# Kernel tuning notes

Hardware: AMD Instinct MI355X
Metric: run time of the kernel (lower is better)

## Reference

```python
import jax, jax.numpy as jnp
import numpy as np

B, N, C = 16, 1024, 768
D = 512
DEPTH = 4
K = 3
HP = WP = 32
A_EPS = 1e-4
POW_MIN = 1e-20
LN_EPS = 1e-5


def setup_inputs() -> dict:
    key = jax.random.key(0)
    ks = jax.random.split(key, 20)
    inp = {
        "tokens": jax.random.normal(ks[0], (B, N, C), dtype=jnp.float32),
        "in_proj_w": jax.random.normal(ks[1], (C, D), dtype=jnp.float32) * 0.02,
        "in_proj_b": jnp.zeros((D,), dtype=jnp.float32),
        "blk_norm_w": jnp.ones((DEPTH, D), dtype=jnp.float32),
        "blk_norm_b": jnp.zeros((DEPTH, D), dtype=jnp.float32),
        "blk_inp_w": jax.random.normal(ks[2], (DEPTH, D, 2 * D), dtype=jnp.float32) * 0.02,
        "blk_inp_b": jnp.zeros((DEPTH, 2 * D), dtype=jnp.float32),
        "blk_conv_w": jax.random.normal(ks[3], (DEPTH, K, K, 1, D), dtype=jnp.float32) * 0.1,
        "blk_conv_b": jnp.zeros((DEPTH, D), dtype=jnp.float32),
        "blk_a_logit": jax.random.normal(ks[4], (DEPTH, D), dtype=jnp.float32) * 0.1,
        "blk_b": jnp.ones((DEPTH, D), dtype=jnp.float32) + jax.random.normal(ks[5], (DEPTH, D), dtype=jnp.float32) * 0.02,
        "blk_c": jnp.ones((DEPTH, D), dtype=jnp.float32) + jax.random.normal(ks[6], (DEPTH, D), dtype=jnp.float32) * 0.02,
        "blk_d": jnp.ones((DEPTH, D), dtype=jnp.float32) + jax.random.normal(ks[7], (DEPTH, D), dtype=jnp.float32) * 0.02,
        "blk_out_w": jax.random.normal(ks[8], (DEPTH, D, D), dtype=jnp.float32) * 0.02,
        "blk_out_b": jnp.zeros((DEPTH, D), dtype=jnp.float32),
        "out_norm_w": jnp.ones((D,), dtype=jnp.float32),
        "out_norm_b": jnp.zeros((D,), dtype=jnp.float32),
    }
    return inp


def _layernorm(x, w, b):
    mu = jnp.mean(x, axis=-1, keepdims=True)
    var = jnp.var(x, axis=-1, keepdims=True)
    return (x - mu) * jax.lax.rsqrt(var + LN_EPS) * w + b


def _ssm_scan(x, a_logit, bb, cc, dd):
    # x: (B', L, D)   s_t = a s_{t-1} + b x_t ; y_t = c s_t + d x_t  (log-domain cumsum form)
    L = x.shape[1]
    a = jnp.clip(jax.nn.sigmoid(a_logit), A_EPS, 1.0 - A_EPS)
    t = jnp.arange(L, dtype=jnp.float32)
    a_pow = jnp.maximum(jnp.exp(t[:, None] * jnp.log(a)[None, :]), POW_MIN)  # (L, D)
    u = x * bb  # (B', L, D)
    r = jnp.cumsum(u / a_pow[None], axis=1)
    s = r * a_pow[None]
    return s * cc + x * dd


def _scan2d(x, a_logit, bb, cc, dd):
    # x: (B, H, W, D); bidirectional row-major + col-major scans, averaged
    Bb, H, W, Dd = x.shape
    L = H * W
    seq_row = x.reshape(Bb, L, Dd)
    seq_col = jnp.transpose(x, (0, 2, 1, 3)).reshape(Bb, L, Dd)
    seqs = jnp.concatenate([seq_row, seq_col], axis=0)            # (2B, L, D)
    all_seqs = jnp.concatenate([seqs, seqs[:, ::-1]], axis=0)     # (4B, L, D)
    y2 = _ssm_scan(all_seqs, a_logit, bb, cc, dd)
    y_f, y_rev = jnp.split(y2, 2, axis=0)
    y = 0.5 * (y_f + y_rev[:, ::-1])
    y_row, y_col = jnp.split(y, 2, axis=0)
    y_row_map = y_row.reshape(Bb, H, W, Dd)
    y_col_map = jnp.transpose(y_col.reshape(Bb, W, H, Dd), (0, 2, 1, 3))
    return 0.5 * (y_row_map + y_col_map)


def _dwconv_silu(x, kernel, bias):
    # x: (B,H,W,D); kernel: (K,K,1,D) depthwise; SAME padding (odd k)
    y = jax.lax.conv_general_dilated(
        x, kernel, window_strides=(1, 1), padding="SAME",
        feature_group_count=x.shape[-1],
        dimension_numbers=("NHWC", "HWIO", "NHWC"))
    return jax.nn.silu(y + bias)


def _block(x, nw, nb, iw, ib, cw, cb, al, sb, sc, sd, ow, ob):
    h = _layernorm(x, nw, nb)
    xg = h @ iw + ib                      # (B,H,W,2D)
    x_in, gate = jnp.split(xg, 2, axis=-1)
    gate = jax.nn.sigmoid(gate)
    u = _dwconv_silu(x_in, cw, cb)
    y = _scan2d(u, al, sb, sc, sd)
    y = (y * gate) @ ow + ob
    return x + y


def reference(tokens, in_proj_w, in_proj_b, blk_norm_w, blk_norm_b, blk_inp_w,
              blk_inp_b, blk_conv_w, blk_conv_b, blk_a_logit, blk_b, blk_c,
              blk_d, blk_out_w, blk_out_b, out_norm_w, out_norm_b):
    x = tokens @ in_proj_w + in_proj_b          # (B, N, D)
    x = x.reshape(B, HP, WP, D)                 # token grid
    for i in range(DEPTH):
        x = _block(x, blk_norm_w[i], blk_norm_b[i], blk_inp_w[i], blk_inp_b[i],
                   blk_conv_w[i], blk_conv_b[i], blk_a_logit[i], blk_b[i],
                   blk_c[i], blk_d[i], blk_out_w[i], blk_out_b[i])
    x = _layernorm(x, out_norm_w, out_norm_b)
    return jnp.mean(x, axis=(1, 2))             # pooled global vector (B, D)
```

## Files before the change

kernel.cpp:

```cpp
#include <hip/hip_runtime.h>
#include <hip/hip_bf16.h>
#include <math.h>

#define NPOS 16384
#define DD   512
#define PP   ((size_t)NPOS * DD)

typedef __bf16 bf16x8 __attribute__((ext_vector_type(8)));
typedef __bf16 bf16x4 __attribute__((ext_vector_type(4)));
typedef float  f32x4  __attribute__((ext_vector_type(4)));

__global__ __launch_bounds__(256, 3) void gemm_bf_k(
    const __bf16* __restrict__ A, const __bf16* __restrict__ Bt,
    const float* __restrict__ bias, const float* __restrict__ res,
    float* __restrict__ C0, __bf16* __restrict__ C1, __bf16* __restrict__ C1b,
    int N, int K, int epi)
{
  __shared__ __bf16 Asm[2][128 * 32];
  __shared__ __bf16 Bsm[2][128 * 32];
  const int tid  = threadIdx.x;
  const int wave = tid >> 6;
  const int lane = tid & 63;
  const int quad = lane >> 4;
  const int l16  = lane & 15;
  const int bm = blockIdx.x * 128;
  const int bn = blockIdx.y * 128;
  const int wm = (wave >> 1) << 6;
  const int wn = (wave & 1) << 6;

  const int r0 = tid >> 2;
  const int r1 = r0 + 64;
  const int sl = (tid & 3) << 3;
  const int ca = (((tid & 3) ^ ((r0 >> 1) & 3)) << 3);

  f32x4 acc[4][4];
  const f32x4 z4 = {0.f, 0.f, 0.f, 0.f};
  #pragma unroll
  for (int i = 0; i < 4; ++i)
    #pragma unroll
    for (int j = 0; j < 4; ++j) acc[i][j] = z4;

  const __bf16* Ab = A  + (size_t)bm * K;
  const __bf16* Bb = Bt + (size_t)bn * K;
  const int nk = K >> 5;

  bf16x8 ar0, ar1, br0, br1;

  #define GLOAD(kb)                                                      \
    {                                                                    \
      const int k0s = (kb) << 5;                                         \
      ar0 = *(const bf16x8*)(Ab + (size_t)r0 * K + k0s + ca);            \
      ar1 = *(const bf16x8*)(Ab + (size_t)r1 * K + k0s + ca);            \
      br0 = *(const bf16x8*)(Bb + (size_t)r0 * K + k0s + ca);            \
      br1 = *(const bf16x8*)(Bb + (size_t)r1 * K + k0s + ca);            \
    }
  #define DSWRITE(buf)                                                   \
    {                                                                    \
      *(bf16x8*)(&Asm[buf][r0 * 32 + sl]) = ar0;                         \
      *(bf16x8*)(&Asm[buf][r1 * 32 + sl]) = ar1;                         \
      *(bf16x8*)(&Bsm[buf][r0 * 32 + sl]) = br0;                         \
      *(bf16x8*)(&Bsm[buf][r1 * 32 + sl]) = br1;                         \
    }

  GLOAD(0)
  DSWRITE(0)
  if (nk > 1) GLOAD(1)
  __syncthreads();

  int cur = 0;
  for (int kb = 0; kb < nk; ++kb) {
    bf16x8 af[4], bg[4];
    #pragma unroll
    for (int i = 0; i < 4; ++i) {
      int m = wm + i * 16 + l16;
      af[i] = *(const bf16x8*)(&Asm[cur][m * 32 + ((quad ^ ((m >> 1) & 3)) << 3)]);
    }
    #pragma unroll
    for (int j = 0; j < 4; ++j) {
      int n = wn + j * 16 + l16;
      bg[j] = *(const bf16x8*)(&Bsm[cur][n * 32 + ((quad ^ ((n >> 1) & 3)) << 3)]);
    }
    #pragma unroll
    for (int i = 0; i < 4; ++i)
      #pragma unroll
      for (int j = 0; j < 4; ++j)
        acc[i][j] = __builtin_amdgcn_mfma_f32_16x16x32_bf16(af[i], bg[j], acc[i][j], 0, 0, 0);
    if (kb + 1 < nk) {
      DSWRITE(cur ^ 1)
      if (kb + 2 < nk) GLOAD(kb + 2)
    }
    __syncthreads();
    cur ^= 1;
  }
  #undef GLOAD
  #undef DSWRITE

  const bool dosig = (epi == 1) && (bn >= 512);
  #pragma unroll
  for (int j = 0; j < 4; ++j) {
    const int col = wn + j * 16 + l16;
    const float bv = bias[bn + col];
    #pragma unroll
    for (int i = 0; i < 4; ++i) {
      const int row0 = bm + wm + i * 16 + quad * 4;
      #pragma unroll
      for (int r = 0; r < 4; ++r) {
        float v = acc[i][j][r] + bv;
        if (epi == 1) {
          if (dosig) {
            v = 1.f / (1.f + expf(-v));
            C1[(size_t)(row0 + r) * 512 + (bn - 512) + col] = (__bf16)v;
          } else {
            C1b[(size_t)(row0 + r) * 512 + bn + col] = (__bf16)v;
          }
        } else {
          size_t off = (size_t)(row0 + r) * N + bn + col;
          if (epi == 2) v += res[off];
          C0[off] = v;
        }
      }
    }
  }
}

__global__ __launch_bounds__(256) void cvt_k(const float* __restrict__ s, __bf16* __restrict__ d)
{
  size_t i = ((size_t)blockIdx.x * 256 + threadIdx.x) * 8;
  float4 a = *(const float4*)(s + i);
  float4 b = *(const float4*)(s + i + 4);
  bf16x8 v;
  v[0] = (__bf16)a.x; v[1] = (__bf16)a.y; v[2] = (__bf16)a.z; v[3] = (__bf16)a.w;
  v[4] = (__bf16)b.x; v[5] = (__bf16)b.y; v[6] = (__bf16)b.z; v[7] = (__bf16)b.w;
  *(bf16x8*)(d + i) = v;
}

__global__ __launch_bounds__(256) void tr_k(const float* __restrict__ src, __bf16* __restrict__ dst,
                                            int K, int N, size_t sstr, size_t dstr)
{
  __shared__ float t[32][33];
  const float* s = src + blockIdx.z * sstr;
  __bf16* d = dst + blockIdx.z * dstr;
  int n0 = blockIdx.x * 32, k0 = blockIdx.y * 32;
  int tx = threadIdx.x & 31, ty = threadIdx.x >> 5;
  #pragma unroll
  for (int i = 0; i < 4; ++i)
    t[ty + i * 8][tx] = s[(size_t)(k0 + ty + i * 8) * N + n0 + tx];
  __syncthreads();
  #pragma unroll
  for (int i = 0; i < 4; ++i)
    d[(size_t)(n0 + ty + i * 8) * K + k0 + tx] = (__bf16)t[tx][ty + i * 8];
}

__global__ __launch_bounds__(256) void ln_k(const float* __restrict__ x, const float* __restrict__ w,
                                            const float* __restrict__ bv, __bf16* __restrict__ out)
{
  int gw = (blockIdx.x * 256 + threadIdx.x) >> 6;
  int lane = threadIdx.x & 63;
  const float* xp = x + ((size_t)gw << 9) + lane * 8;
  float4 u0 = *(const float4*)xp;
  float4 u1 = *(const float4*)(xp + 4);
  float v[8] = {u0.x,u0.y,u0.z,u0.w,u1.x,u1.y,u1.z,u1.w};
  float s = 0.f;
  #pragma unroll
  for (int j = 0; j < 8; ++j) s += v[j];
  #pragma unroll
  for (int off = 32; off; off >>= 1) s += __shfl_xor(s, off, 64);
  float mu = s * (1.f/512.f);
  float q = 0.f;
  #pragma unroll
  for (int j = 0; j < 8; ++j) { float d = v[j] - mu; q += d*d; }
  #pragma unroll
  for (int off = 32; off; off >>= 1) q += __shfl_xor(q, off, 64);
  float rstd = rsqrtf(q * (1.f/512.f) + 1e-5f);
  int dch = lane * 8;
  float4 w0 = *(const float4*)(w + dch),  w1 = *(const float4*)(w + dch + 4);
  float4 b0 = *(const float4*)(bv + dch), b1 = *(const float4*)(bv + dch + 4);
  float wv[8] = {w0.x,w0.y,w0.z,w0.w,w1.x,w1.y,w1.z,w1.w};
  float bb[8] = {b0.x,b0.y,b0.z,b0.w,b1.x,b1.y,b1.z,b1.w};
  bf16x8 ov;
  #pragma unroll
  for (int j = 0; j < 8; ++j) ov[j] = (__bf16)((v[j] - mu) * rstd * wv[j] + bb[j]);
  *(bf16x8*)(out + ((size_t)gw << 9) + dch) = ov;
}

__device__ __forceinline__ float sig_a(float al) {
  float a = 1.f / (1.f + expf(-al));
  return fminf(fmaxf(a, 1e-4f), 1.f - 1e-4f);
}

__global__ __launch_bounds__(512, 2) void scan2d_k(
    const __bf16* __restrict__ xin, const float* __restrict__ cw, const float* __restrict__ cb,
    const float* __restrict__ alog, const float* __restrict__ bvec, const float* __restrict__ cvec,
    const float* __restrict__ dvec, const __bf16* __restrict__ gate, __bf16* __restrict__ yo)
{
  __shared__ __bf16 T[32768];
  __shared__ __bf16 Y[32768];
  __shared__ float  S[4][32][32];
  const int tid = threadIdx.x;
  const int cg  = blockIdx.x;
  const int b   = blockIdx.y;
  const int ch  = tid & 31;
  const int c0  = tid >> 5;
  const int c1  = c0 + 16;
  const int d   = (cg << 5) + ch;

  const float a   = sig_a(alog[d]);
  const float lna = logf(a);
  const float ia  = 1.f / a;
  const float bb  = bvec[d];
  const float sc  = 0.25f * cvec[d];
  const float dd  = dvec[d];

  const __bf16* ub = xin + ((size_t)b << 19) + (cg << 5);

  #pragma unroll
  for (int i = 0; i < 8; ++i) {
    int flat = (tid + i * 512) << 3;
    int pos = flat >> 5;
    int c8  = flat & 31;
    *(bf16x8*)(T + flat) = *(const bf16x8*)(ub + (size_t)pos * 512 + c8);
  }
  float w00 = cw[(0 << 9) + d], w01 = cw[(1 << 9) + d], w02 = cw[(2 << 9) + d];
  float w10 = cw[(3 << 9) + d], w11 = cw[(4 << 9) + d], w12 = cw[(5 << 9) + d];
  float w20 = cw[(6 << 9) + d], w21 = cw[(7 << 9) + d], w22 = cw[(8 << 9) + d];
  const float cbv = cb[d];
  const float A0f = expf((float)(c0 << 5) * lna),        R0f = expf((float)(c0 << 5) * -lna);
  const float A1f = expf((float)(c1 << 5) * lna),        R1f = expf((float)(c1 << 5) * -lna);
  const float A0b = expf((float)((31 - c0) << 5) * lna), R0b = expf((float)((31 - c0) << 5) * -lna);
  const float A1b = expf((float)((31 - c1) << 5) * lna), R1b = expf((float)((31 - c1) << 5) * -lna);
  __syncthreads();

  {
    const bool up0 = (c0 > 0);
    const bool dn1 = (c0 < 15);
    float a0 = 0.f, a1 = 0.f, a2 = 0.f, f0 = 0.f, f1 = 0.f, f2 = 0.f;
    float b0 = up0 ? (float)T[(((c0 - 1) << 5)) * 32 + ch] : 0.f;
    float b1 =        (float)T[((c0 << 5)) * 32 + ch];
    float b2 =        (float)T[(((c0 + 1) << 5)) * 32 + ch];
    float g0 =        (float)T[(((c1 - 1) << 5)) * 32 + ch];
    float g1 =        (float)T[((c1 << 5)) * 32 + ch];
    float g2 = dn1 ? (float)T[(((c1 + 1) << 5)) * 32 + ch] : 0.f;
    #pragma unroll 4
    for (int ww = 0; ww < 32; ++ww) {
      float e0 = 0.f, e1 = 0.f, e2 = 0.f, i0 = 0.f, i1 = 0.f, i2 = 0.f;
      if (ww < 31) {
        e0 = up0 ? (float)T[(((c0 - 1) << 5) + ww + 1) * 32 + ch] : 0.f;
        e1 =        (float)T[((c0 << 5) + ww + 1) * 32 + ch];
        e2 =        (float)T[(((c0 + 1) << 5) + ww + 1) * 32 + ch];
        i0 =        (float)T[(((c1 - 1) << 5) + ww + 1) * 32 + ch];
        i1 =        (float)T[((c1 << 5) + ww + 1) * 32 + ch];
        i2 = dn1 ? (float)T[(((c1 + 1) << 5) + ww + 1) * 32 + ch] : 0.f;
      }
      float acc0 = cbv, acc1 = cbv;
      acc0 = fmaf(a0, w00, acc0); acc0 = fmaf(b0, w01, acc0); acc0 = fmaf(e0, w02, acc0);
      acc0 = fmaf(a1, w10, acc0); acc0 = fmaf(b1, w11, acc0); acc0 = fmaf(e1, w12, acc0);
      acc0 = fmaf(a2, w20, acc0); acc0 = fmaf(b2, w21, acc0); acc0 = fmaf(e2, w22, acc0);
      acc1 = fmaf(f0, w00, acc1); acc1 = fmaf(g0, w01, acc1); acc1 = fmaf(i0, w02, acc1);
      acc1 = fmaf(f1, w10, acc1); acc1 = fmaf(g1, w11, acc1); acc1 = fmaf(i1, w12, acc1);
      acc1 = fmaf(f2, w20, acc1); acc1 = fmaf(g2, w21, acc1); acc1 = fmaf(i2, w22, acc1);
      acc0 = acc0 / (1.f + expf(-acc0));
      acc1 = acc1 / (1.f + expf(-acc1));
      Y[((c0 << 5) + ww) * 32 + ch] = (__bf16)acc0;
      Y[((c1 << 5) + ww) * 32 + ch] = (__bf16)acc1;
      a0 = b0; a1 = b1; a2 = b2; b0 = e0; b1 = e1; b2 = e2;
      f0 = g0; f1 = g1; f2 = g2; g0 = i0; g1 = i1; g2 = i2;
    }
  }
  __syncthreads();

  #define STEP(r_, uu_, apr_, rp_)                                 \
    { float rr_ = (apr_ < 1e-20f) ? 1e20f : rp_;                   \
      r_ = fmaf((uu_) * bb, rr_, r_); }

  {
    float p0 = A0f, q0 = R0f, p0B = A0b, q0B = R0b;
    float p1 = A1f, q1 = R1f, p1B = A1b, q1B = R1b;
    float s0 = 0.f, s1 = 0.f, s2 = 0.f, s3 = 0.f;
    float s4 = 0.f, s5 = 0.f, s6 = 0.f, s7 = 0.f;
    #pragma unroll 4
    for (int j = 0; j < 32; ++j) {
      float u0rf = (float)Y[((c0 << 5) + j) * 32 + ch];
      float u0rb = (float)Y[((c0 << 5) + (31 - j)) * 32 + ch];
      float u0cf = (float)Y[((j << 5) | c0) * 32 + ch];
      float u0cb = (float)Y[(((31 - j) << 5) | c0) * 32 + ch];
      float u1rf = (float)Y[((c1 << 5) + j) * 32 + ch];
      float u1rb = (float)Y[((c1 << 5) + (31 - j)) * 32 + ch];
      float u1cf = (float)Y[((j << 5) | c1) * 32 + ch];
      float u1cb = (float)Y[(((31 - j) << 5) | c1) * 32 + ch];
      STEP(s0, u0rf, p0, q0)  STEP(s2, u0cf, p0, q0)
      STEP(s1, u0rb, p0B, q0B) STEP(s3, u0cb, p0B, q0B)
      STEP(s4, u1rf, p1, q1)  STEP(s6, u1cf, p1, q1)
      STEP(s5, u1rb, p1B, q1B) STEP(s7, u1cb, p1B, q1B)
      p0 *= a; q0 *= ia; p0B *= a; q0B *= ia;
      p1 *= a; q1 *= ia; p1B *= a; q1B *= ia;
    }
    S[0][c0][ch] = s0; S[1][c0][ch] = s1; S[2][c0][ch] = s2; S[3][c0][ch] = s3;
    S[0][c1][ch] = s4; S[1][c1][ch] = s5; S[2][c1][ch] = s6; S[3][c1][ch] = s7;
  }
  __syncthreads();

  if (tid < 128) {
    int arr = tid >> 5, ch2 = tid & 31;
    float run = 0.f;
    if ((arr & 1) == 0) {
      #pragma unroll 4
      for (int cc = 0; cc < 32; ++cc) { float v = S[arr][cc][ch2]; S[arr][cc][ch2] = run; run += v; }
    } else {
      #pragma unroll 4
      for (int cc = 31; cc >= 0; --cc) { float v = S[arr][cc][ch2]; S[arr][cc][ch2] = run; run += v; }
    }
  }
  __syncthreads();

  {
    float r0 = S[2][c0][ch], r1 = S[2][c1][ch];
    float p0 = A0f, q0 = R0f, p1 = A1f, q1 = R1f;
    #pragma unroll 4
    for (int j = 0; j < 32; ++j) {
      int i0 = ((j << 5) | c0) * 32 + ch, i1 = ((j << 5) | c1) * 32 + ch;
      float u0 = (float)Y[i0], u1 = (float)Y[i1];
      float ap0 = fmaxf(p0, 1e-20f), ap1 = fmaxf(p1, 1e-20f);
      STEP(r0, u0, p0, q0) STEP(r1, u1, p1, q1)
      T[i0] = (__bf16)(r0 * ap0);
      T[i1] = (__bf16)(r1 * ap1);
      p0 *= a; q0 *= ia; p1 *= a; q1 *= ia;
    }
  }
  {
    float r0 = S[3][c0][ch], r1 = S[3][c1][ch];
    float p0 = A0b, q0 = R0b, p1 = A1b, q1 = R1b;
    #pragma unroll 4
    for (int j = 31; j >= 0; --j) {
      int i0 = ((j << 5) | c0) * 32 + ch, i1 = ((j << 5) | c1) * 32 + ch;
      float u0 = (float)Y[i0], u1 = (float)Y[i1];
      float ap0 = fmaxf(p0, 1e-20f), ap1 = fmaxf(p1, 1e-20f);
      STEP(r0, u0, p0, q0) STEP(r1, u1, p1, q1)
      T[i0] = (__bf16)(sc * ((float)T[i0] + r0 * ap0));
      T[i1] = (__bf16)(sc * ((float)T[i1] + r1 * ap1));
      p0 *= a; q0 *= ia; p1 *= a; q1 *= ia;
    }
  }
  __syncthreads();

  {
    float r0 = S[0][c0][ch], r1 = S[0][c1][ch];
    float p0 = A0f, q0 = R0f, p1 = A1f, q1 = R1f;
    #pragma unroll 4
    for (int j = 0; j < 32; ++j) {
      int i0 = ((c0 << 5) + j) * 32 + ch, i1 = ((c1 << 5) + j) * 32 + ch;
      float u0 = (float)Y[i0], u1 = (float)Y[i1];
      float ap0 = fmaxf(p0, 1e-20f), ap1 = fmaxf(p1, 1e-20f);
      STEP(r0, u0, p0, q0) STEP(r1, u1, p1, q1)
      T[i0] = (__bf16)((float)T[i0] + sc * (r0 * ap0));
      T[i1] = (__bf16)((float)T[i1] + sc * (r1 * ap1));
      p0 *= a; q0 *= ia; p1 *= a; q1 *= ia;
    }
  }
  {
    const __bf16* gb = gate + ((size_t)b << 19) + (cg << 5) + ch;
    __bf16* yb = yo + ((size_t)b << 19) + (cg << 5) + ch;
    float r0 = S[1][c0][ch], r1 = S[1][c1][ch];
    float p0 = A0b, q0 = R0b, p1 = A1b, q1 = R1b;
    #pragma unroll 4
    for (int j = 31; j >= 0; --j) {
      int pp0 = (c0 << 5) + j, pp1 = (c1 << 5) + j;
      int i0 = pp0 * 32 + ch, i1 = pp1 * 32 + ch;
      float u0 = (float)Y[i0], u1 = (float)Y[i1];
      float ap0 = fmaxf(p0, 1e-20f), ap1 = fmaxf(p1, 1e-20f);
      STEP(r0, u0, p0, q0) STEP(r1, u1, p1, q1)
      float y0 = (float)T[i0] + sc * (r0 * ap0) + dd * u0;
      float y1 = (float)T[i1] + sc * (r1 * ap1) + dd * u1;
      yb[(size_t)pp0 * 512] = (__bf16)(y0 * (float)gb[(size_t)pp0 * 512]);
      yb[(size_t)pp1 * 512] = (__bf16)(y1 * (float)gb[(size_t)pp1 * 512]);
      p0 *= a; q0 *= ia; p1 *= a; q1 *= ia;
    }
  }
  #undef STEP
}

__global__ __launch_bounds__(256) void reduce_k(const __bf16* __restrict__ hn, float* __restrict__ out)
{
  __shared__ float part[4][64];
  int l = threadIdx.x & 63;
  int q = threadIdx.x >> 6;
  int d = blockIdx.y * 64 + l;
  int b = blockIdx.x;
  const __bf16* p = hn + ((size_t)b << 19) + d + ((size_t)(q * 256) << 9);
  float s0 = 0.f, s1 = 0.f, s2 = 0.f, s3 = 0.f;
  for (int t = 0; t < 256; t += 4) {
    s0 += (float)p[(size_t)(t+0) << 9];
    s1 += (float)p[(size_t)(t+1) << 9];
    s2 += (float)p[(size_t)(t+2) << 9];
    s3 += (float)p[(size_t)(t+3) << 9];
  }
  part[q][l] = (s0 + s1) + (s2 + s3);
  __syncthreads();
  if (threadIdx.x < 64)
    out[b * 512 + d] = (part[0][l] + part[1][l] + part[2][l] + part[3][l]) * (1.f / 1024.f);
}

extern "C" void kernel_launch(void* const* d_in, const int* in_sizes, int n_in,
                              void* d_out, int out_size, void* d_ws, size_t ws_size,
                              hipStream_t stream)
{
  const float* tokens = (const float*)d_in[0];
  const float* in_w   = (const float*)d_in[1];
  const float* in_b   = (const float*)d_in[2];
  const float* nw     = (const float*)d_in[3];
  const float* nb     = (const float*)d_in[4];
  const float* iw     = (const float*)d_in[5];
  const float* ib     = (const float*)d_in[6];
  const float* cw     = (const float*)d_in[7];
  const float* cb     = (const float*)d_in[8];
  const float* al     = (const float*)d_in[9];
  const float* bbv    = (const float*)d_in[10];
  const float* ccv    = (const float*)d_in[11];
  const float* ddv    = (const float*)d_in[12];
  const float* ow     = (const float*)d_in[13];
  const float* obv    = (const float*)d_in[14];
  const float* onw    = (const float*)d_in[15];
  const float* onb    = (const float*)d_in[16];

  float*  x     = (float*)d_ws;
  __bf16* hy16  = (__bf16*)(x + PP);
  __bf16* xin16 = hy16 + PP;
  __bf16* g16   = xin16 + PP;
  __bf16* iwT   = g16 + PP;
  __bf16* owT   = iwT + (size_t)4 * 1024 * 512;
  __bf16* tb16  = owT + (size_t)4 * 512 * 512;
  __bf16* inwT  = xin16;

  cvt_k<<<6144, 256, 0, stream>>>(tokens, tb16);
  tr_k<<<dim3(16, 24, 1), 256, 0, stream>>>(in_w, inwT, 768, 512, 0, 0);
  tr_k<<<dim3(32, 16, 4), 256, 0, stream>>>(iw, iwT, 512, 1024, (size_t)512*1024, (size_t)1024*512);
  tr_k<<<dim3(16, 16, 4), 256, 0, stream>>>(ow, owT, 512, 512, (size_t)512*512, (size_t)512*512);

  gemm_bf_k<<<dim3(128, 4), 256, 0, stream>>>(tb16, inwT, in_b, nullptr, x, nullptr, nullptr,
                                              512, 768, 0);

  for (int i = 0; i < 4; ++i) {
    ln_k<<<4096, 256, 0, stream>>>(x, nw + i*512, nb + i*512, hy16);
    gemm_bf_k<<<dim3(128, 8), 256, 0, stream>>>(hy16, iwT + (size_t)i*1024*512, ib + i*1024,
                                                nullptr, nullptr, g16, xin16, 1024, 512, 1);
    scan2d_k<<<dim3(16, 16), 512, 0, stream>>>(xin16, cw + i*9*512, cb + i*512,
                                               al + i*512, bbv + i*512, ccv + i*512,
                                               ddv + i*512, g16, hy16);
    gemm_bf_k<<<dim3(128, 4), 256, 0, stream>>>(hy16, owT + (size_t)i*512*512, obv + i*512,
                                                x, x, nullptr, nullptr, 512, 512, 2);
  }

  ln_k<<<4096, 256, 0, stream>>>(x, onw, onb, hy16);
  reduce_k<<<dim3(16, 8), 256, 0, stream>>>(hy16, (float*)d_out);
}
```

Before: 654.3 us.

## Rewrite GEMM with direct-to-LDS loads, triple buffering, larger tiles and XCD-aware block mapping

Replaces the 128x128 register-staged double-buffered GEMM with a 512-thread kernel using 128x256 or 256x256 tiles. Tiles go straight from global memory to LDS via global_load_lds across a three-stage buffer ring, with explicit vmcnt waits and raw barriers. It also raises MFMA priority with setprio and remaps block indices so neighbouring tiles share an XCD. The aim is better data reuse and overlap of loads with MFMA, at the cost of more LDS use, lower occupancy, and fragile hand-counted waits.

```diff
diff --git a/kernel.cpp b/kernel.cpp
--- a/kernel.cpp
+++ b/kernel.cpp
@@ -7,93 +7,137 @@
 #define PP   ((size_t)NPOS * DD)
 
 typedef __bf16 bf16x8 __attribute__((ext_vector_type(8)));
-typedef __bf16 bf16x4 __attribute__((ext_vector_type(4)));
 typedef float  f32x4  __attribute__((ext_vector_type(4)));
 
-__global__ __launch_bounds__(256, 3) void gemm_bf_k(
+__device__ __forceinline__ void gload16(const __bf16* g, __bf16* l) {
+  __builtin_amdgcn_global_load_lds((__attribute__((address_space(1))) void*)(g),
+                                   (__attribute__((address_space(3))) void*)(l), 16, 0, 0);
+}
+__device__ __forceinline__ void wait_vm0() { asm volatile("s_waitcnt vmcnt(0)" ::: "memory"); }
+__device__ __forceinline__ void wait_vm3() { asm volatile("s_waitcnt vmcnt(3)" ::: "memory"); }
+__device__ __forceinline__ void wait_vm4() { asm volatile("s_waitcnt vmcnt(4)" ::: "memory"); }
+
+template<int BM>
+__global__ __launch_bounds__(512, 2) void gemm8p_k(
     const __bf16* __restrict__ A, const __bf16* __restrict__ Bt,
     const float* __restrict__ bias, const float* __restrict__ res,
     float* __restrict__ C0, __bf16* __restrict__ C1, __bf16* __restrict__ C1b,
     int N, int K, int epi)
 {
-  __shared__ __bf16 Asm[2][128 * 32];
-  __shared__ __bf16 Bsm[2][128 * 32];
+  constexpr int PH = BM / 128;
+  __shared__ __bf16 Asm[3][BM * 32];
+  __shared__ __bf16 Bsm[3][256 * 32];
+
   const int tid  = threadIdx.x;
-  const int wave = tid >> 6;
+  const int w    = tid >> 6;
   const int lane = tid & 63;
   const int quad = lane >> 4;
   const int l16  = lane & 15;
-  const int bm = blockIdx.x * 128;
-  const int bn = blockIdx.y * 128;
-  const int wm = (wave >> 1) << 6;
-  const int wn = (wave & 1) << 6;
-
-  const int r0 = tid >> 2;
-  const int r1 = r0 + 64;
-  const int sl = (tid & 3) << 3;
-  const int ca = (((tid & 3) ^ ((r0 >> 1) & 3)) << 3);
-
-  f32x4 acc[4][4];
-  const f32x4 z4 = {0.f, 0.f, 0.f, 0.f};
-  #pragma unroll
-  for (int i = 0; i < 4; ++i)
-    #pragma unroll
-    for (int j = 0; j < 4; ++j) acc[i][j] = z4;
+  const int wm   = (w >> 2) * (BM / 2);
+  const int wn   = (w & 3) * 64;
+
+  const int nwg = gridDim.x;
+  const int cpx = nwg >> 3;
+  const int lin = (blockIdx.x & 7) * cpx + (blockIdx.x >> 3);
+  const int nbn = N >> 8;
+  const int sh  = (nbn == 4) ? 2 : 1;
+  const int mt  = lin >> sh;
+  const int ntc = lin & (nbn - 1);
+  const int bm  = mt * BM;
+  const int bn  = ntc << 8;
 
   const __bf16* Ab = A  + (size_t)bm * K;
   const __bf16* Bb = Bt + (size_t)bn * K;
   const int nk = K >> 5;
 
-  bf16x8 ar0, ar1, br0, br1;
-
-  #define GLOAD(kb)                                                      \
-    {                                                                    \
-      const int k0s = (kb) << 5;                                         \
-      ar0 = *(const bf16x8*)(Ab + (size_t)r0 * K + k0s + ca);            \
-      ar1 = *(const bf16x8*)(Ab + (size_t)r1 * K + k0s + ca);            \
-      br0 = *(const bf16x8*)(Bb + (size_t)r0 * K + k0s + ca);            \
-      br1 = *(const bf16x8*)(Bb + (size_t)r1 * K + k0s + ca);            \
-    }
-  #define DSWRITE(buf)                                                   \
-    {                                                                    \
-      *(bf16x8*)(&Asm[buf][r0 * 32 + sl]) = ar0;                         \
-      *(bf16x8*)(&Asm[buf][r1 * 32 + sl]) = ar1;                         \
-      *(bf16x8*)(&Bsm[buf][r0 * 32 + sl]) = br0;                         \
-      *(bf16x8*)(&Bsm[buf][r1 * 32 + sl]) = br1;                         \
-    }
-
-  GLOAD(0)
-  DSWRITE(0)
-  if (nk > 1) GLOAD(1)
-  __syncthreads();
+  f32x4 acc[4 * PH][4];
+  #pragma unroll
+  for (int i = 0; i < 4 * PH; ++i)
+    #pragma unroll
+    for (int j = 0; j < 4; ++j) acc[i][j] = (f32x4){0.f, 0.f, 0.f, 0.f};
+
+  #define STG_A(tile, buf, k2) {                                               \
+    const int ch_ = tid + (k2) * 512;                                          \
+    const int r_ = ch_ >> 2, c_ = ch_ & 3;                                     \
+    gload16(Ab + (size_t)r_ * K + ((tile) << 5) + ((c_ ^ ((r_ >> 1) & 3)) << 3),\
+            &Asm[buf][ch_ << 3]);                                              \
+  }
+  #define STG_B(tile, buf, k2) {                                               \
+    const int ch_ = tid + (k2) * 512;                                          \
+    const int r_ = ch_ >> 2, c_ = ch_ & 3;                                     \
+    gload16(Bb + (size_t)r_ * K + ((tile) << 5) + ((c_ ^ ((r_ >> 1) & 3)) << 3),\
+            &Bsm[buf][ch_ << 3]);                                              \
+  }
+
+  STG_A(0, 0, 0)
+  if constexpr (BM == 256) STG_A(0, 0, 1)
+  STG_B(0, 0, 0)
+  STG_B(0, 0, 1)
+  STG_A(1, 1, 0)
+  if constexpr (BM == 256) STG_A(1, 1, 1)
+  STG_B(1, 1, 0)
+  STG_B(1, 1, 1)
+  if constexpr (BM == 256) { wait_vm4(); } else { wait_vm3(); }
+  __builtin_amdgcn_s_barrier();
 
   int cur = 0;
-  for (int kb = 0; kb < nk; ++kb) {
-    bf16x8 af[4], bg[4];
+  for (int t = 0; t < nk; ++t) {
+    const int nx2 = (cur == 0) ? 2 : cur - 1;
+    const bool st = (t + 2 < nk);
+    bf16x8 af[4], bfr[4];
+
     #pragma unroll
     for (int i = 0; i < 4; ++i) {
-      int m = wm + i * 16 + l16;
+      const int m = wm + i * 16 + l16;
       af[i] = *(const bf16x8*)(&Asm[cur][m * 32 + ((quad ^ ((m >> 1) & 3)) << 3)]);
     }
     #pragma unroll
     for (int j = 0; j < 4; ++j) {
-      int n = wn + j * 16 + l16;
-      bg[j] = *(const bf16x8*)(&Bsm[cur][n * 32 + ((quad ^ ((n >> 1) & 3)) << 3)]);
-    }
+      const int n = wn + j * 16 + l16;
+      bfr[j] = *(const bf16x8*)(&Bsm[cur][n * 32 + ((quad ^ ((n >> 1) & 3)) << 3)]);
+    }
+    if (st) {
+      STG_A(t + 2, nx2, 0)
+      STG_B(t + 2, nx2, 0)
+      if constexpr (BM == 128) STG_B(t + 2, nx2, 1)
+    }
+    __builtin_amdgcn_s_barrier();
+    __builtin_amdgcn_s_setprio(1);
     #pragma unroll
     for (int i = 0; i < 4; ++i)
       #pragma unroll
       for (int j = 0; j < 4; ++j)
-        acc[i][j] = __builtin_amdgcn_mfma_f32_16x16x32_bf16(af[i], bg[j], acc[i][j], 0, 0, 0);
-    if (kb + 1 < nk) {
-      DSWRITE(cur ^ 1)
-      if (kb + 2 < nk) GLOAD(kb + 2)
-    }
-    __syncthreads();
-    cur ^= 1;
-  }
-  #undef GLOAD
-  #undef DSWRITE
+        acc[i][j] = __builtin_amdgcn_mfma_f32_16x16x32_bf16(af[i], bfr[j], acc[i][j], 0, 0, 0);
+    __builtin_amdgcn_s_setprio(0);
+
+    if constexpr (BM == 256) {
+      __builtin_amdgcn_s_barrier();
+      #pragma unroll
+      for (int i = 0; i < 4; ++i) {
+        const int m = wm + 64 + i * 16 + l16;
+        af[i] = *(const bf16x8*)(&Asm[cur][m * 32 + ((quad ^ ((m >> 1) & 3)) << 3)]);
+      }
+      if (st) {
+        STG_A(t + 2, nx2, 1)
+        STG_B(t + 2, nx2, 1)
+      }
+      __builtin_amdgcn_s_barrier();
+      __builtin_amdgcn_s_setprio(1);
+      #pragma unroll
+      for (int i = 0; i < 4; ++i)
+        #pragma unroll
+        for (int j = 0; j < 4; ++j)
+          acc[4 + i][j] = __builtin_amdgcn_mfma_f32_16x16x32_bf16(af[i], bfr[j], acc[4 + i][j], 0, 0, 0);
+      __builtin_amdgcn_s_setprio(0);
+    }
+
+    if (st) { if constexpr (BM == 256) { wait_vm4(); } else { wait_vm3(); } }
+    else    { wait_vm0(); }
+    __builtin_amdgcn_s_barrier();
+    cur = (cur == 2) ? 0 : cur + 1;
+  }
+  #undef STG_A
+  #undef STG_B
 
   const bool dosig = (epi == 1) && (bn >= 512);
   #pragma unroll
@@ -101,8 +145,8 @@
     const int col = wn + j * 16 + l16;
     const float bv = bias[bn + col];
     #pragma unroll
-    for (int i = 0; i < 4; ++i) {
-      const int row0 = bm + wm + i * 16 + quad * 4;
+    for (int i = 0; i < 4 * PH; ++i) {
+      const int row0 = bm + wm + (i >> 2) * 64 + (i & 3) * 16 + quad * 4;
       #pragma unroll
       for (int r = 0; r < 4; ++r) {
         float v = acc[i][j][r] + bv;
@@ -435,18 +479,18 @@
   tr_k<<<dim3(32, 16, 4), 256, 0, stream>>>(iw, iwT, 512, 1024, (size_t)512*1024, (size_t)1024*512);
   tr_k<<<dim3(16, 16, 4), 256, 0, stream>>>(ow, owT, 512, 512, (size_t)512*512, (size_t)512*512);
 
-  gemm_bf_k<<<dim3(128, 4), 256, 0, stream>>>(tb16, inwT, in_b, nullptr, x, nullptr, nullptr,
-                                              512, 768, 0);
+  gemm8p_k<128><<<256, 512, 0, stream>>>(tb16, inwT, in_b, nullptr, x, nullptr, nullptr,
+                                         512, 768, 0);
 
   for (int i = 0; i < 4; ++i) {
     ln_k<<<4096, 256, 0, stream>>>(x, nw + i*512, nb + i*512, hy16);
-    gemm_bf_k<<<dim3(128, 8), 256, 0, stream>>>(hy16, iwT + (size_t)i*1024*512, ib + i*1024,
-                                                nullptr, nullptr, g16, xin16, 1024, 512, 1);
+    gemm8p_k<256><<<256, 512, 0, stream>>>(hy16, iwT + (size_t)i*1024*512, ib + i*1024,
+                                           nullptr, nullptr, g16, xin16, 1024, 512, 1);
     scan2d_k<<<dim3(16, 16), 512, 0, stream>>>(xin16, cw + i*9*512, cb + i*512,
                                                al + i*512, bbv + i*512, ccv + i*512,
                                                ddv + i*512, g16, hy16);
-    gemm_bf_k<<<dim3(128, 4), 256, 0, stream>>>(hy16, owT + (size_t)i*512*512, obv + i*512,
-                                                x, x, nullptr, nullptr, 512, 512, 2);
+    gemm8p_k<128><<<256, 512, 0, stream>>>(hy16, owT + (size_t)i*512*512, obv + i*512,
+                                           x, x, nullptr, nullptr, 512, 512, 2);
   }
 
   ln_k<<<4096, 256, 0, stream>>>(x, onw, onb, hy16);
```

Measured after the change: 677.4 us. +3.5%, slower.
